# Kernel optimization log

Hardware: AMD Instinct MI355X
Metric: run time of the kernel (lower is better)

Reference implementation:

```python
import jax, jax.numpy as jnp
import numpy as np

EMBED_DIM = 1024
NUM_HEADS = 16
HEAD_DIM = EMBED_DIM // NUM_HEADS


def _rope_tables(seq_len, dim, dtype):
    # inv_freq over even indices of head_dim
    inv_freq = 1.0 / (10000.0 ** (jnp.arange(0, dim, 2, dtype=jnp.float32) / dim))
    t = jnp.arange(seq_len, dtype=jnp.float32)
    freqs = jnp.einsum('i,j->ij', t, inv_freq)            # [S, dim/2]
    emb = jnp.concatenate([freqs, freqs], axis=-1)        # [S, dim]
    return jnp.cos(emb).astype(dtype)[None], jnp.sin(emb).astype(dtype)[None]  # [1,S,dim]


def _rotate_half(x):
    x1, x2 = jnp.split(x, 2, axis=-1)
    return jnp.concatenate([-x2, x1], axis=-1)


def _apply_rope(x, cos, sin):
    return x * cos + _rotate_half(x) * sin


def setup_inputs() -> dict:
    key = jax.random.key(0)
    ks = jax.random.split(key, 9)
    S, B, E = 2048, 2, EMBED_DIM
    sc = 1.0 / np.sqrt(E)
    inp = {
        'query': jax.random.normal(ks[0], (S, B, E), jnp.float32),
        'Wq': jax.random.normal(ks[1], (E, E), jnp.float32) * sc,
        'bq': jnp.zeros((E,), jnp.float32),
        'Wk': jax.random.normal(ks[2], (E, E), jnp.float32) * sc,
        'bk': jnp.zeros((E,), jnp.float32),
        'Wv': jax.random.normal(ks[3], (E, E), jnp.float32) * sc,
        'bv': jnp.zeros((E,), jnp.float32),
        'Wo': jax.random.normal(ks[4], (E, E), jnp.float32) * sc,
        'bo': jnp.zeros((E,), jnp.float32),
    }
    return inp


def reference(query, Wq, bq, Wk, bk, Wv, bv, Wo, bo):
    tgt_len, bsz, E = query.shape
    H, hd = NUM_HEADS, HEAD_DIM
    scaling = hd ** (-0.5)

    # self-attention projections (torch Linear: x @ W.T + b)
    q = (query @ Wq.T + bq) * scaling
    k = query @ Wk.T + bk
    v = query @ Wv.T + bv

    # [S, B, E] -> [B*H, S, hd]
    def to_heads(x):
        return x.reshape(tgt_len, bsz * H, hd).transpose(1, 0, 2)

    q, k, v = to_heads(q), to_heads(k), to_heads(v)

    cos, sin = _rope_tables(tgt_len, hd, q.dtype)  # [1,S,hd]
    q = _apply_rope(q, cos, sin)
    k = _apply_rope(k, cos, sin)

    attn_weights = jnp.einsum('bqd,bkd->bqk', q, k)       # [B*H, S, S]
    attn_probs = jax.nn.softmax(attn_weights, axis=-1)
    attn = jnp.einsum('bqk,bkd->bqd', attn_probs, v)      # [B*H, S, hd]

    attn = attn.transpose(1, 0, 2).reshape(tgt_len, bsz, E)
    return attn @ Wo.T + bo
```

## Files before the change

kernel.cpp:

```cpp
#include <hip/hip_runtime.h>
#include <hip/hip_bf16.h>


typedef short shortx8 __attribute__((ext_vector_type(8)));
typedef float floatx4 __attribute__((ext_vector_type(4)));

#define S_LEN 2048
#define BATCH 2
#define EMB 1024
#define NH 16
#define HD 64
#define BH 32
#define MROWS 4096
#define HEAD_STRIDE (S_LEN*HD)

#define QSCALE 0.1803368801111204f

#if __has_builtin(__builtin_amdgcn_exp2f)
#define EXP2(x) __builtin_amdgcn_exp2f(x)
#else
#define EXP2(x) exp2f(x)
#endif

__device__ __forceinline__ float b2f(unsigned short u) {
    union { unsigned int i; float f; } v; v.i = ((unsigned int)u) << 16; return v.f;
}
__device__ __forceinline__ unsigned short f2b(float f) {
    union { float f; unsigned int i; } v; v.f = f;
    unsigned int x = v.i;
    return (unsigned short)((x + 0x7fffu + ((x >> 16) & 1u)) >> 16);
}
__device__ __forceinline__ unsigned short f2b_fast(float f) {
    union { float f; unsigned int i; } v; v.f = f;
    return (unsigned short)((v.i + 0x8000u) >> 16);
}
__device__ __forceinline__ shortx8 cvt8(const float* p) {
    floatx4 a = *(const floatx4*)p;
    floatx4 b = *(const floatx4*)(p + 4);
    shortx8 r;
    r[0] = (short)f2b(a[0]); r[1] = (short)f2b(a[1]);
    r[2] = (short)f2b(a[2]); r[3] = (short)f2b(a[3]);
    r[4] = (short)f2b(b[0]); r[5] = (short)f2b(b[1]);
    r[6] = (short)f2b(b[2]); r[7] = (short)f2b(b[3]);
    return r;
}
__device__ __forceinline__ void g2l16(const unsigned short* g, unsigned short* l) {
    __builtin_amdgcn_global_load_lds(
        (const __attribute__((address_space(1))) unsigned int*)(const void*)g,
        (__attribute__((address_space(3))) unsigned int*)(void*)l, 16, 0, 0);
}

__global__ __launch_bounds__(256) void prep(
    const float* __restrict__ X,
    const float* __restrict__ Wq, const float* __restrict__ Wk,
    const float* __restrict__ Wv,
    unsigned short* __restrict__ Xb, unsigned short* __restrict__ Wb,
    float* __restrict__ rtab)
{
    const int g = blockIdx.x * 256 + threadIdx.x;
    if (g < 65536) {
        const int s = g >> 5, j = g & 31;
        const float inv = expf(-(float)j * (9.210340371976184f / 32.0f));
        const float ang = (float)s * inv;
        rtab[s * 64 + j]      = cosf(ang);
        rtab[s * 64 + 32 + j] = sinf(ang);
    } else if (g < 458752) {
        const int h = g - 65536;
        const int seg = h >> 17;
        const int idx = (h & 131071) * 8;
        const float* W = (seg == 0) ? Wq : (seg == 1) ? Wk : Wv;
        *(shortx8*)&Wb[seg * 1048576 + idx] = cvt8(&W[idx]);
    } else {
        const int idx = (g - 458752) * 8;
        *(shortx8*)&Xb[idx] = cvt8(&X[idx]);
    }
}

__global__ __launch_bounds__(256) void cvt_w1(
    const float* __restrict__ Wo, unsigned short* __restrict__ Wb)
{
    const int g = blockIdx.x * 256 + threadIdx.x;
    const int idx = g * 8;
    *(shortx8*)&Wb[idx] = cvt8(&Wo[idx]);
}

__device__ __forceinline__ void qkv_epilogue(
    floatx4 (&acc)[4][4], int mat, int m0, int nn0, int wm, int wn,
    int qm, int quad, const float* bias, const float* rtab,
    unsigned short* dst)
{
    if (mat == 2) {
#pragma unroll
        for (int i = 0; i < 4; i++) {
#pragma unroll
            for (int j = 0; j < 4; j++) {
                const int colg = nn0 + wn + j * 16 + qm;
                const float bv_ = bias[colg];
                const int h = colg >> 6, d = colg & 63;
#pragma unroll
                for (int r = 0; r < 4; r++) {
                    const int rowg = m0 + wm + i * 16 + quad * 4 + r;
                    const int s = rowg >> 1, b = rowg & 1;
                    dst[((b * NH + h) * HD + d) * S_LEN + s] = f2b(acc[i][j][r] + bv_);
                }
            }
        }
    } else {
        const float scale = (mat == 0) ? QSCALE : 1.0f;
#pragma unroll
        for (int i = 0; i < 4; i++) {
#pragma unroll
            for (int jp = 0; jp < 2; jp++) {
                const int c1 = nn0 + wn + jp * 16 + qm;
                const float b1 = bias[c1], b2 = bias[c1 + 32];
                const int h = c1 >> 6;
                const int d1 = c1 & 63;
#pragma unroll
                for (int r = 0; r < 4; r++) {
                    const int rowg = m0 + wm + i * 16 + quad * 4 + r;
                    const int s = rowg >> 1, b = rowg & 1;
                    const float cs = rtab[s * 64 + d1];
                    const float sn = rtab[s * 64 + d1 + 32];
                    const float x1 = (acc[i][jp][r] + b1) * scale;
                    const float x2 = (acc[i][jp + 2][r] + b2) * scale;
                    unsigned short* base = &dst[((b * NH + h) * S_LEN + s) * HD];
                    base[d1]      = f2b(x1 * cs - x2 * sn);
                    base[d1 + 32] = f2b(x2 * cs + x1 * sn);
                }
            }
        }
    }
}

__global__ __launch_bounds__(256) void qkv_gemm_gl(
    const unsigned short* __restrict__ Xb,
    const unsigned short* __restrict__ Wb,
    const float* __restrict__ bq, const float* __restrict__ bk,
    const float* __restrict__ bv,
    const float* __restrict__ rtab,
    unsigned short* __restrict__ Qh, unsigned short* __restrict__ Kh,
    unsigned short* __restrict__ Vt)
{
    __shared__ unsigned short At[128 * 64];
    __shared__ unsigned short Bt[128 * 64];

    const int tid  = threadIdx.x;
    const int wave = tid >> 6, lane = tid & 63;
    const int wm = (wave >> 1) * 64, wn = (wave & 1) * 64;
    const int qm = lane & 15, quad = lane >> 4;

    const int m0  = blockIdx.x * 128;
    const int n0g = blockIdx.y * 128;
    const int mat = n0g >> 10;
    const int nn0 = n0g & 1023;

    const unsigned short* W = Wb + (size_t)mat * 1048576;
    const float* bias = (mat == 0) ? bq : (mat == 1) ? bk : bv;
    unsigned short* dst = (mat == 0) ? Qh : (mat == 1) ? Kh : Vt;

    floatx4 acc[4][4] = {};

    const int xs = qm & 7;

    for (int k0 = 0; k0 < EMB; k0 += 64) {
#pragma unroll
        for (int c = 0; c < 4; c++) {
            const int e   = (c * 256 + tid) * 8;
            const int row = e >> 6;
            const int gcol = (((e >> 3) & 7) ^ (row & 7)) * 8;
            g2l16(&Xb[(m0 + row) * EMB + k0 + gcol], &At[e]);
            g2l16(&W[(nn0 + row) * EMB + k0 + gcol], &Bt[e]);
        }
        __syncthreads();

#pragma unroll
        for (int kk = 0; kk < 2; kk++) {
            shortx8 a[4], b[4];
#pragma unroll
            for (int i = 0; i < 4; i++)
                a[i] = *(shortx8*)&At[(wm + i * 16 + qm) * 64 + (((kk * 4 + quad) ^ xs) * 8)];
#pragma unroll
            for (int j = 0; j < 4; j++)
                b[j] = *(shortx8*)&Bt[(wn + j * 16 + qm) * 64 + (((kk * 4 + quad) ^ xs) * 8)];
#pragma unroll
            for (int i = 0; i < 4; i++)
#pragma unroll
                for (int j = 0; j < 4; j++)
                    acc[i][j] = __builtin_amdgcn_mfma_f32_16x16x32_bf16(a[i], b[j], acc[i][j], 0, 0, 0);
        }
        __syncthreads();
    }

    qkv_epilogue(acc, mat, m0, nn0, wm, wn, qm, quad, bias, rtab, dst);
}

#define LDB 72

__global__ __launch_bounds__(256) void qkv_gemm_fb(
    const float* __restrict__ X,
    const unsigned short* __restrict__ Wb,
    const float* __restrict__ bq, const float* __restrict__ bk,
    const float* __restrict__ bv,
    const float* __restrict__ rtab,
    unsigned short* __restrict__ Qh, unsigned short* __restrict__ Kh,
    unsigned short* __restrict__ Vt)
{
    __shared__ unsigned short At[128 * LDB];
    __shared__ unsigned short Bt[128 * LDB];

    const int tid  = threadIdx.x;
    const int wave = tid >> 6, lane = tid & 63;
    const int wm = (wave >> 1) * 64, wn = (wave & 1) * 64;
    const int qm = lane & 15, quad = lane >> 4;

    const int m0  = blockIdx.x * 128;
    const int n0g = blockIdx.y * 128;
    const int mat = n0g >> 10;
    const int nn0 = n0g & 1023;

    const unsigned short* W = Wb + (size_t)mat * 1048576;
    const float* bias = (mat == 0) ? bq : (mat == 1) ? bk : bv;
    unsigned short* dst = (mat == 0) ? Qh : (mat == 1) ? Kh : Vt;

    const int r0 = tid >> 3;
    const int ko = (tid & 7) * 8;

    floatx4 acc[4][4] = {};

    for (int k0 = 0; k0 < EMB; k0 += 64) {
#pragma unroll
        for (int c = 0; c < 4; c++) {
            const int row = r0 + 32 * c;
            *(shortx8*)&At[row * LDB + ko] = cvt8(&X[(m0 + row) * EMB + k0 + ko]);
            *(shortx8*)&Bt[row * LDB + ko] = *(const shortx8*)&W[(nn0 + row) * EMB + k0 + ko];
        }
        __syncthreads();

#pragma unroll
        for (int kk = 0; kk < 2; kk++) {
            shortx8 a[4], b[4];
#pragma unroll
            for (int i = 0; i < 4; i++)
                a[i] = *(shortx8*)&At[(wm + i * 16 + qm) * LDB + kk * 32 + quad * 8];
#pragma unroll
            for (int j = 0; j < 4; j++)
                b[j] = *(shortx8*)&Bt[(wn + j * 16 + qm) * LDB + kk * 32 + quad * 8];
#pragma unroll
            for (int i = 0; i < 4; i++)
#pragma unroll
                for (int j = 0; j < 4; j++)
                    acc[i][j] = __builtin_amdgcn_mfma_f32_16x16x32_bf16(a[i], b[j], acc[i][j], 0, 0, 0);
        }
        __syncthreads();
    }

    qkv_epilogue(acc, mat, m0, nn0, wm, wn, qm, quad, bias, rtab, dst);
}

#define LDK 72
#define LDV 136

__global__ __launch_bounds__(512) void attn_kernel(
    unsigned short* Qh,
    const unsigned short* __restrict__ Kh,
    const unsigned short* __restrict__ Vt)
{
    __shared__ unsigned short ldsK[128 * LDK];
    __shared__ unsigned short ldsVT[64 * LDV];
    __shared__ unsigned short ldsP[8 * 16 * LDV];

    const int tid  = threadIdx.x;
    const int wave = tid >> 6, lane = tid & 63;
    const int qm = lane & 15, quad = lane >> 4;
    const int bh = blockIdx.y;
    const int qrow = blockIdx.x * 128 + wave * 16;

    unsigned short* Qp = Qh + bh * HEAD_STRIDE;
    const unsigned short* Kp = Kh + bh * HEAD_STRIDE;
    const unsigned short* Vp = Vt + bh * HEAD_STRIDE;

    const shortx8 aq0 = *(const shortx8*)&Qp[(qrow + qm) * HD + quad * 8];
    const shortx8 aq1 = *(const shortx8*)&Qp[(qrow + qm) * HD + 32 + quad * 8];

    floatx4 od[4] = {};
    float l_part[4] = {0.f, 0.f, 0.f, 0.f};

    unsigned short* myP = &ldsP[wave * 16 * LDV];

    const int kr = tid >> 3;
    const int ko = (tid & 7) * 8;
    const int vr = tid >> 4;
    const int vo = (tid & 15) * 8;

    for (int kt = 0; kt < S_LEN / 128; kt++) {
        const int kbase = kt * 128;
#pragma unroll
        for (int c = 0; c < 2; c++) {
            *(shortx8*)&ldsK[(kr + 64 * c) * LDK + ko] =
                *(const shortx8*)&Kp[(kbase + kr + 64 * c) * HD + ko];
            *(shortx8*)&ldsVT[(vr + 32 * c) * LDV + vo] =
                *(const shortx8*)&Vp[(vr + 32 * c) * S_LEN + kbase + vo];
        }
        __syncthreads();

        floatx4 sc[8];
#pragma unroll
        for (int nt = 0; nt < 8; nt++) {
            const int krow = nt * 16 + qm;
            const shortx8 b0 = *(shortx8*)&ldsK[krow * LDK + quad * 8];
            const shortx8 b1 = *(shortx8*)&ldsK[krow * LDK + 32 + quad * 8];
            floatx4 a = {};
            a = __builtin_amdgcn_mfma_f32_16x16x32_bf16(aq0, b0, a, 0, 0, 0);
            a = __builtin_amdgcn_mfma_f32_16x16x32_bf16(aq1, b1, a, 0, 0, 0);
            sc[nt] = a;
        }

#pragma unroll
        for (int nt = 0; nt < 8; nt++)
#pragma unroll
            for (int r = 0; r < 4; r++)
                sc[nt][r] = EXP2(sc[nt][r]);
#pragma unroll
        for (int r = 0; r < 4; r++) {
            float t0 = (sc[0][r] + sc[1][r]) + (sc[2][r] + sc[3][r]);
            float t1 = (sc[4][r] + sc[5][r]) + (sc[6][r] + sc[7][r]);
            l_part[r] += t0 + t1;
        }

#pragma unroll
        for (int nt = 0; nt < 8; nt++)
#pragma unroll
            for (int r = 0; r < 4; r++)
                myP[(quad * 4 + r) * LDV + nt * 16 + qm] = f2b_fast(sc[nt][r]);

        shortx8 ap[4];
#pragma unroll
        for (int kc = 0; kc < 4; kc++)
            ap[kc] = *(shortx8*)&myP[qm * LDV + kc * 32 + quad * 8];
#pragma unroll
        for (int dt = 0; dt < 4; dt++) {
            const int d = dt * 16 + qm;
#pragma unroll
            for (int kc = 0; kc < 4; kc++) {
                const shortx8 vb = *(shortx8*)&ldsVT[d * LDV + kc * 32 + quad * 8];
                od[dt] = __builtin_amdgcn_mfma_f32_16x16x32_bf16(ap[kc], vb, od[dt], 0, 0, 0);
            }
        }
        __syncthreads();
    }

    float inv_l[4];
#pragma unroll
    for (int r = 0; r < 4; r++) {
        float s = l_part[r];
        for (int off = 1; off < 16; off <<= 1) s += __shfl_xor(s, off, 64);
        inv_l[r] = 1.0f / s;
    }

#pragma unroll
    for (int r = 0; r < 4; r++) {
        const int rq = qrow + quad * 4 + r;
#pragma unroll
        for (int dt = 0; dt < 4; dt++) {
            const int d = dt * 16 + qm;
            Qp[rq * HD + d] = f2b(od[dt][r] * inv_l[r]);
        }
    }
}

#define LDA 40

__global__ __launch_bounds__(256) void out_gemm(
    const unsigned short* __restrict__ O,
    const unsigned short* __restrict__ Wob, const float* __restrict__ bo,
    float* __restrict__ out)
{
    __shared__ unsigned short At[128 * LDA];
    __shared__ unsigned short Bt[128 * LDA];

    const int tid  = threadIdx.x;
    const int wave = tid >> 6, lane = tid & 63;
    const int wm = (wave >> 1) * 64, wn = (wave & 1) * 64;
    const int qm = lane & 15, quad = lane >> 4;
    const int m0 = blockIdx.x * 128;
    const int n0 = blockIdx.y * 128;

    const int r0 = tid >> 2;
    const int ko = (tid & 3) * 8;

    floatx4 acc[4][4] = {};

    for (int k0 = 0; k0 < EMB; k0 += 32) {
        const int k = k0 + ko;
        const int m1 = m0 + r0, m2 = m0 + r0 + 64;
        *(shortx8*)&At[r0 * LDA + ko] =
            *(const shortx8*)&O[(((m1 & 1) * NH + (k >> 6)) * S_LEN + (m1 >> 1)) * HD + (k & 63)];
        *(shortx8*)&At[(r0 + 64) * LDA + ko] =
            *(const shortx8*)&O[(((m2 & 1) * NH + (k >> 6)) * S_LEN + (m2 >> 1)) * HD + (k & 63)];
        *(shortx8*)&Bt[r0 * LDA + ko]        = *(const shortx8*)&Wob[(n0 + r0) * EMB + k];
        *(shortx8*)&Bt[(r0 + 64) * LDA + ko] = *(const shortx8*)&Wob[(n0 + r0 + 64) * EMB + k];
        __syncthreads();

        shortx8 a[4], b[4];
#pragma unroll
        for (int i = 0; i < 4; i++) a[i] = *(shortx8*)&At[(wm + i * 16 + qm) * LDA + quad * 8];
#pragma unroll
        for (int j = 0; j < 4; j++) b[j] = *(shortx8*)&Bt[(wn + j * 16 + qm) * LDA + quad * 8];
#pragma unroll
        for (int i = 0; i < 4; i++)
#pragma unroll
            for (int j = 0; j < 4; j++)
                acc[i][j] = __builtin_amdgcn_mfma_f32_16x16x32_bf16(a[i], b[j], acc[i][j], 0, 0, 0);
        __syncthreads();
    }

#pragma unroll
    for (int i = 0; i < 4; i++) {
#pragma unroll
        for (int j = 0; j < 4; j++) {
            const int colg = n0 + wn + j * 16 + qm;
            const float bv_ = bo[colg];
#pragma unroll
            for (int r = 0; r < 4; r++) {
                const int rowg = m0 + wm + i * 16 + quad * 4 + r;
                out[rowg * EMB + colg] = acc[i][j][r] + bv_;
            }
        }
    }
}

extern "C" void kernel_launch(void* const* d_in, const int* in_sizes, int n_in,
                              void* d_out, int out_size, void* d_ws, size_t ws_size,
                              hipStream_t stream) {
    const float* X  = (const float*)d_in[0];
    const float* Wq = (const float*)d_in[1];
    const float* bq = (const float*)d_in[2];
    const float* Wk = (const float*)d_in[3];
    const float* bk = (const float*)d_in[4];
    const float* Wv = (const float*)d_in[5];
    const float* bv = (const float*)d_in[6];
    const float* Wo = (const float*)d_in[7];
    const float* bo = (const float*)d_in[8];
    float* out = (float*)d_out;

    unsigned short* ws = (unsigned short*)d_ws;
    unsigned short* Vt  = ws;
    unsigned short* Qh  = ws + (size_t)BH * HEAD_STRIDE;
    unsigned short* Xb  = ws + (size_t)2 * BH * HEAD_STRIDE;
    unsigned short* Kh  = (unsigned short*)d_out;
    unsigned short* Wb  = (unsigned short*)d_out + 4194304;
    float*          Rt  = (float*)d_out + 3670016;
    unsigned short* Wob = ws;

    const bool use_xb = ws_size >= (size_t)24 * 1024 * 1024;

    prep<<<dim3(use_xb ? 3840 : 1792), 256, 0, stream>>>(X, Wq, Wk, Wv, Xb, Wb, Rt);

    if (use_xb)
        qkv_gemm_gl<<<dim3(MROWS / 128, 3 * EMB / 128), 256, 0, stream>>>(
            Xb, Wb, bq, bk, bv, Rt, Qh, Kh, Vt);
    else
        qkv_gemm_fb<<<dim3(MROWS / 128, 3 * EMB / 128), 256, 0, stream>>>(
            X, Wb, bq, bk, bv, Rt, Qh, Kh, Vt);

    attn_kernel<<<dim3(S_LEN / 128, BH), 512, 0, stream>>>(Qh, Kh, Vt);
    cvt_w1<<<dim3(131072 / 256), 256, 0, stream>>>(Wo, Wob);
    out_gemm<<<dim3(MROWS / 128, EMB / 128), 256, 0, stream>>>(Qh, Wob, bo, out);
}
```

Before: 225.2 us.

## Prefetch K/V tiles into registers in attention; fuse Wo conversion into out GEMM

The attention loop now prefetches the next K/V tile from global memory into registers while the current tile is computed, so load latency can overlap with the MFMA work (unrolled by two). The separate cvt_w1 kernel is removed, and the output GEMM converts fp32 Wo to bf16 inline while loading, with the K step widened from 32 to 64. This saves a launch and a round trip of the converted weight through memory, at the cost of more register pressure and redundant Wo conversion across the M-blocks.

```diff
diff --git a/kernel.cpp b/kernel.cpp
--- a/kernel.cpp
+++ b/kernel.cpp
@@ -76,14 +76,6 @@
     }
 }
 
-__global__ __launch_bounds__(256) void cvt_w1(
-    const float* __restrict__ Wo, unsigned short* __restrict__ Wb)
-{
-    const int g = blockIdx.x * 256 + threadIdx.x;
-    const int idx = g * 8;
-    *(shortx8*)&Wb[idx] = cvt8(&Wo[idx]);
-}
-
 __device__ __forceinline__ void qkv_epilogue(
     floatx4 (&acc)[4][4], int mat, int m0, int nn0, int wm, int wn,
     int qm, int quad, const float* bias, const float* rtab,
@@ -260,6 +252,54 @@
 #define LDK 72
 #define LDV 136
 
+__device__ __forceinline__ void attn_tile_compute(
+    const unsigned short* ldsK, const unsigned short* ldsVT,
+    unsigned short* myP, shortx8 aq0, shortx8 aq1,
+    int qm, int quad, floatx4 (&od)[4], float (&l_part)[4])
+{
+    floatx4 sc[8];
+#pragma unroll
+    for (int nt = 0; nt < 8; nt++) {
+        const int krow = nt * 16 + qm;
+        const shortx8 b0 = *(const shortx8*)&ldsK[krow * LDK + quad * 8];
+        const shortx8 b1 = *(const shortx8*)&ldsK[krow * LDK + 32 + quad * 8];
+        floatx4 a = {};
+        a = __builtin_amdgcn_mfma_f32_16x16x32_bf16(aq0, b0, a, 0, 0, 0);
+        a = __builtin_amdgcn_mfma_f32_16x16x32_bf16(aq1, b1, a, 0, 0, 0);
+        sc[nt] = a;
+    }
+#pragma unroll
+    for (int nt = 0; nt < 8; nt++)
+#pragma unroll
+        for (int r = 0; r < 4; r++)
+            sc[nt][r] = EXP2(sc[nt][r]);
+#pragma unroll
+    for (int r = 0; r < 4; r++) {
+        float t0 = (sc[0][r] + sc[1][r]) + (sc[2][r] + sc[3][r]);
+        float t1 = (sc[4][r] + sc[5][r]) + (sc[6][r] + sc[7][r]);
+        l_part[r] += t0 + t1;
+    }
+#pragma unroll
+    for (int nt = 0; nt < 8; nt++)
+#pragma unroll
+        for (int r = 0; r < 4; r++)
+            myP[(quad * 4 + r) * LDV + nt * 16 + qm] = f2b_fast(sc[nt][r]);
+
+    shortx8 ap[4];
+#pragma unroll
+    for (int kc = 0; kc < 4; kc++)
+        ap[kc] = *(const shortx8*)&myP[qm * LDV + kc * 32 + quad * 8];
+#pragma unroll
+    for (int dt = 0; dt < 4; dt++) {
+        const int d = dt * 16 + qm;
+#pragma unroll
+        for (int kc = 0; kc < 4; kc++) {
+            const shortx8 vb = *(const shortx8*)&ldsVT[d * LDV + kc * 32 + quad * 8];
+            od[dt] = __builtin_amdgcn_mfma_f32_16x16x32_bf16(ap[kc], vb, od[dt], 0, 0, 0);
+        }
+    }
+}
+
 __global__ __launch_bounds__(512) void attn_kernel(
     unsigned short* Qh,
     const unsigned short* __restrict__ Kh,
@@ -292,60 +332,43 @@
     const int vr = tid >> 4;
     const int vo = (tid & 15) * 8;
 
-    for (int kt = 0; kt < S_LEN / 128; kt++) {
-        const int kbase = kt * 128;
-#pragma unroll
-        for (int c = 0; c < 2; c++) {
-            *(shortx8*)&ldsK[(kr + 64 * c) * LDK + ko] =
-                *(const shortx8*)&Kp[(kbase + kr + 64 * c) * HD + ko];
-            *(shortx8*)&ldsVT[(vr + 32 * c) * LDV + vo] =
-                *(const shortx8*)&Vp[(vr + 32 * c) * S_LEN + kbase + vo];
-        }
-        __syncthreads();
-
-        floatx4 sc[8];
-#pragma unroll
-        for (int nt = 0; nt < 8; nt++) {
-            const int krow = nt * 16 + qm;
-            const shortx8 b0 = *(shortx8*)&ldsK[krow * LDK + quad * 8];
-            const shortx8 b1 = *(shortx8*)&ldsK[krow * LDK + 32 + quad * 8];
-            floatx4 a = {};
-            a = __builtin_amdgcn_mfma_f32_16x16x32_bf16(aq0, b0, a, 0, 0, 0);
-            a = __builtin_amdgcn_mfma_f32_16x16x32_bf16(aq1, b1, a, 0, 0, 0);
-            sc[nt] = a;
-        }
-
-#pragma unroll
-        for (int nt = 0; nt < 8; nt++)
-#pragma unroll
-            for (int r = 0; r < 4; r++)
-                sc[nt][r] = EXP2(sc[nt][r]);
-#pragma unroll
-        for (int r = 0; r < 4; r++) {
-            float t0 = (sc[0][r] + sc[1][r]) + (sc[2][r] + sc[3][r]);
-            float t1 = (sc[4][r] + sc[5][r]) + (sc[6][r] + sc[7][r]);
-            l_part[r] += t0 + t1;
-        }
-
-#pragma unroll
-        for (int nt = 0; nt < 8; nt++)
-#pragma unroll
-            for (int r = 0; r < 4; r++)
-                myP[(quad * 4 + r) * LDV + nt * 16 + qm] = f2b_fast(sc[nt][r]);
-
-        shortx8 ap[4];
-#pragma unroll
-        for (int kc = 0; kc < 4; kc++)
-            ap[kc] = *(shortx8*)&myP[qm * LDV + kc * 32 + quad * 8];
-#pragma unroll
-        for (int dt = 0; dt < 4; dt++) {
-            const int d = dt * 16 + qm;
-#pragma unroll
-            for (int kc = 0; kc < 4; kc++) {
-                const shortx8 vb = *(shortx8*)&ldsVT[d * LDV + kc * 32 + quad * 8];
-                od[dt] = __builtin_amdgcn_mfma_f32_16x16x32_bf16(ap[kc], vb, od[dt], 0, 0, 0);
-            }
-        }
+    shortx8 ka0, ka1, va0, va1;
+    shortx8 kb0, kb1, vb0, vb1;
+
+    ka0 = *(const shortx8*)&Kp[kr * HD + ko];
+    ka1 = *(const shortx8*)&Kp[(kr + 64) * HD + ko];
+    va0 = *(const shortx8*)&Vp[vr * S_LEN + vo];
+    va1 = *(const shortx8*)&Vp[(vr + 32) * S_LEN + vo];
+
+    for (int kt = 0; kt < S_LEN / 128; kt += 2) {
+        *(shortx8*)&ldsK[kr * LDK + ko]         = ka0;
+        *(shortx8*)&ldsK[(kr + 64) * LDK + ko]  = ka1;
+        *(shortx8*)&ldsVT[vr * LDV + vo]        = va0;
+        *(shortx8*)&ldsVT[(vr + 32) * LDV + vo] = va1;
+        __syncthreads();
+        {
+            const int kb = (kt + 1) * 128;
+            kb0 = *(const shortx8*)&Kp[(kb + kr) * HD + ko];
+            kb1 = *(const shortx8*)&Kp[(kb + kr + 64) * HD + ko];
+            vb0 = *(const shortx8*)&Vp[vr * S_LEN + kb + vo];
+            vb1 = *(const shortx8*)&Vp[(vr + 32) * S_LEN + kb + vo];
+        }
+        attn_tile_compute(ldsK, ldsVT, myP, aq0, aq1, qm, quad, od, l_part);
+        __syncthreads();
+
+        *(shortx8*)&ldsK[kr * LDK + ko]         = kb0;
+        *(shortx8*)&ldsK[(kr + 64) * LDK + ko]  = kb1;
+        *(shortx8*)&ldsVT[vr * LDV + vo]        = vb0;
+        *(shortx8*)&ldsVT[(vr + 32) * LDV + vo] = vb1;
+        __syncthreads();
+        if (kt + 2 < S_LEN / 128) {
+            const int kb = (kt + 2) * 128;
+            ka0 = *(const shortx8*)&Kp[(kb + kr) * HD + ko];
+            ka1 = *(const shortx8*)&Kp[(kb + kr + 64) * HD + ko];
+            va0 = *(const shortx8*)&Vp[vr * S_LEN + kb + vo];
+            va1 = *(const shortx8*)&Vp[(vr + 32) * S_LEN + kb + vo];
+        }
+        attn_tile_compute(ldsK, ldsVT, myP, aq0, aq1, qm, quad, od, l_part);
         __syncthreads();
     }
 
@@ -368,15 +391,13 @@
     }
 }
 
-#define LDA 40
-
 __global__ __launch_bounds__(256) void out_gemm(
     const unsigned short* __restrict__ O,
-    const unsigned short* __restrict__ Wob, const float* __restrict__ bo,
+    const float* __restrict__ Wo, const float* __restrict__ bo,
     float* __restrict__ out)
 {
-    __shared__ unsigned short At[128 * LDA];
-    __shared__ unsigned short Bt[128 * LDA];
+    __shared__ unsigned short At[128 * LDB];
+    __shared__ unsigned short Bt[128 * LDB];
 
     const int tid  = threadIdx.x;
     const int wave = tid >> 6, lane = tid & 63;
@@ -385,32 +406,38 @@
     const int m0 = blockIdx.x * 128;
     const int n0 = blockIdx.y * 128;
 
-    const int r0 = tid >> 2;
-    const int ko = (tid & 3) * 8;
+    const int r0 = tid >> 3;
+    const int ko = (tid & 7) * 8;
 
     floatx4 acc[4][4] = {};
 
-    for (int k0 = 0; k0 < EMB; k0 += 32) {
+    for (int k0 = 0; k0 < EMB; k0 += 64) {
         const int k = k0 + ko;
-        const int m1 = m0 + r0, m2 = m0 + r0 + 64;
-        *(shortx8*)&At[r0 * LDA + ko] =
-            *(const shortx8*)&O[(((m1 & 1) * NH + (k >> 6)) * S_LEN + (m1 >> 1)) * HD + (k & 63)];
-        *(shortx8*)&At[(r0 + 64) * LDA + ko] =
-            *(const shortx8*)&O[(((m2 & 1) * NH + (k >> 6)) * S_LEN + (m2 >> 1)) * HD + (k & 63)];
-        *(shortx8*)&Bt[r0 * LDA + ko]        = *(const shortx8*)&Wob[(n0 + r0) * EMB + k];
-        *(shortx8*)&Bt[(r0 + 64) * LDA + ko] = *(const shortx8*)&Wob[(n0 + r0 + 64) * EMB + k];
-        __syncthreads();
-
-        shortx8 a[4], b[4];
-#pragma unroll
-        for (int i = 0; i < 4; i++) a[i] = *(shortx8*)&At[(wm + i * 16 + qm) * LDA + quad * 8];
-#pragma unroll
-        for (int j = 0; j < 4; j++) b[j] = *(shortx8*)&Bt[(wn + j * 16 + qm) * LDA + quad * 8];
-#pragma unroll
-        for (int i = 0; i < 4; i++)
+#pragma unroll
+        for (int c = 0; c < 4; c++) {
+            const int row = r0 + 32 * c;
+            const int m = m0 + row;
+            *(shortx8*)&At[row * LDB + ko] =
+                *(const shortx8*)&O[(((m & 1) * NH + (k >> 6)) * S_LEN + (m >> 1)) * HD + (k & 63)];
+            *(shortx8*)&Bt[row * LDB + ko] = cvt8(&Wo[(n0 + row) * EMB + k]);
+        }
+        __syncthreads();
+
+#pragma unroll
+        for (int kk = 0; kk < 2; kk++) {
+            shortx8 a[4], b[4];
+#pragma unroll
+            for (int i = 0; i < 4; i++)
+                a[i] = *(shortx8*)&At[(wm + i * 16 + qm) * LDB + kk * 32 + quad * 8];
 #pragma unroll
             for (int j = 0; j < 4; j++)
-                acc[i][j] = __builtin_amdgcn_mfma_f32_16x16x32_bf16(a[i], b[j], acc[i][j], 0, 0, 0);
+                b[j] = *(shortx8*)&Bt[(wn + j * 16 + qm) * LDB + kk * 32 + quad * 8];
+#pragma unroll
+            for (int i = 0; i < 4; i++)
+#pragma unroll
+                for (int j = 0; j < 4; j++)
+                    acc[i][j] = __builtin_amdgcn_mfma_f32_16x16x32_bf16(a[i], b[j], acc[i][j], 0, 0, 0);
+        }
         __syncthreads();
     }
 
@@ -450,7 +477,6 @@
     unsigned short* Kh  = (unsigned short*)d_out;
     unsigned short* Wb  = (unsigned short*)d_out + 4194304;
     float*          Rt  = (float*)d_out + 3670016;
-    unsigned short* Wob = ws;
 
     const bool use_xb = ws_size >= (size_t)24 * 1024 * 1024;
 
@@ -464,6 +490,5 @@
             X, Wb, bq, bk, bv, Rt, Qh, Kh, Vt);
 
     attn_kernel<<<dim3(S_LEN / 128, BH), 512, 0, stream>>>(Qh, Kh, Vt);
-    cvt_w1<<<dim3(131072 / 256), 256, 0, stream>>>(Wo, Wob);
-    out_gemm<<<dim3(MROWS / 128, EMB / 128), 256, 0, stream>>>(Qh, Wob, bo, out);
-}
+    out_gemm<<<dim3(MROWS / 128, EMB / 128), 256, 0, stream>>>(Qh, Wo, bo, out);
+}
```

Result: slower. 229.7 us (+2.0%).
